# Optimization experiments

Hardware: AMD Instinct MI355X
Metric: run time of the kernel (lower is better)

Reference implementation:

```python
import jax, jax.numpy as jnp
import numpy as np


def setup_inputs() -> dict:
    key = jax.random.key(0)
    inputs = jax.random.normal(key, (32, 56, 56, 256), dtype=jnp.float32)
    return {"inputs": inputs, "n": 48}


def reference(inputs, n):
    # Flatten per batch row: [B, H*W*C]
    B = inputs.shape[0]
    flat = inputs.reshape(B, -1)
    # k-th largest value per row is the threshold
    values, _ = jax.lax.top_k(flat, n)
    thresholds = values[:, -1].reshape(B, 1, 1, 1)
    mask = (inputs >= thresholds).astype(inputs.dtype)
    return inputs * mask
```

## Files before the change

### kernel.cpp

```cpp
#include <hip/hip_runtime.h>
#include <stdint.h>

#define ROWS 32
#define ROW_LEN 802816
#define ROW_LEN4 200704
#define BPR 98
#define F4_PER_BLOCK 2048
#define THREADS 256
#define F4_PER_THREAD 8
#define TG 3.0f
#define BCAP 40
#define CAP_ROW (BPR * BCAP)
#define SLOTS_PT 16

#define OFF_BCNT 501760
#define OFF_THR  514304

__device__ __forceinline__ uint32_t fkey(float x) {
    uint32_t u = __float_as_uint(x);
    return (u & 0x80000000u) ? ~u : (u | 0x80000000u);
}
__device__ __forceinline__ float fkey_inv(uint32_t k) {
    uint32_t u = (k & 0x80000000u) ? (k & 0x7FFFFFFFu) : ~k;
    return __uint_as_float(u);
}

__global__ __launch_bounds__(THREADS) void k_spec(const float* __restrict__ in,
                                                  float* __restrict__ out,
                                                  uint32_t* __restrict__ pos,
                                                  int* __restrict__ bcnt) {
    __shared__ uint32_t lp[BCAP];
    __shared__ int lcnt;
    const int row = blockIdx.x / BPR;
    const int blk = blockIdx.x % BPR;
    if (threadIdx.x == 0) lcnt = 0;
    __syncthreads();
    const size_t base = (size_t)row * ROW_LEN4 + (size_t)blk * F4_PER_BLOCK + threadIdx.x;
    const float4* p = (const float4*)in + base;
    float4* q = (float4*)out + base;
    const float4 z = make_float4(0.f, 0.f, 0.f, 0.f);
#pragma unroll
    for (int v = 0; v < F4_PER_THREAD; ++v) {
        float4 d = p[v * THREADS];
        q[v * THREADS] = z;
        const uint32_t e = (uint32_t)(blk * F4_PER_BLOCK + v * THREADS + threadIdx.x) * 4u;
        if (d.x > TG) { int j = atomicAdd(&lcnt, 1); if (j < BCAP) lp[j] = e + 0u; }
        if (d.y > TG) { int j = atomicAdd(&lcnt, 1); if (j < BCAP) lp[j] = e + 1u; }
        if (d.z > TG) { int j = atomicAdd(&lcnt, 1); if (j < BCAP) lp[j] = e + 2u; }
        if (d.w > TG) { int j = atomicAdd(&lcnt, 1); if (j < BCAP) lp[j] = e + 3u; }
    }
    __syncthreads();
    const int c = lcnt;
    if (threadIdx.x == 0) bcnt[row * BPR + blk] = c;
    const int cc = c < BCAP ? c : BCAP;
    for (int i = threadIdx.x; i < cc; i += THREADS)
        pos[((size_t)row * BPR + blk) * BCAP + i] = lp[i];
}

__device__ __forceinline__ void pick_digit(uint32_t* h, int t, int r,
                                           int* sh_sel, int* sh_rank) {
#pragma unroll
    for (int off = 1; off < 256; off <<= 1) {
        uint32_t v = h[t] + ((t + off < 256) ? h[t + off] : 0u);
        __syncthreads();
        h[t] = v;
        __syncthreads();
    }
    const uint32_t Sd = h[t];
    const uint32_t Sd1 = (t < 255) ? h[t + 1] : 0u;
    if ((int)Sd >= r && (int)Sd1 < r) { *sh_sel = t; *sh_rank = r - (int)Sd1; }
    __syncthreads();
}

__global__ __launch_bounds__(THREADS) void k_sel(const float* __restrict__ in,
                                                 const int* __restrict__ n_ptr,
                                                 const int* __restrict__ bcnt,
                                                 const uint32_t* __restrict__ pos,
                                                 float* __restrict__ out,
                                                 float* __restrict__ thr) {
    __shared__ int lb[BPR];
    __shared__ uint32_t h[256];
    __shared__ int sh_sel, sh_rank, sh_m, sh_bad;
    const int row = blockIdx.x;
    const int t = threadIdx.x;
    const int n = *n_ptr;
    const float* rin = in + (size_t)row * ROW_LEN;
    float* rout = out + (size_t)row * ROW_LEN;

    if (t == 0) { sh_m = 0; sh_bad = 0; }
    __syncthreads();
    {
        int lsum = 0, lbad = 0;
        for (int b = t; b < BPR; b += THREADS) {
            const int c = bcnt[row * BPR + b];
            lbad |= (c > BCAP);
            const int cc = c < BCAP ? c : BCAP;
            lb[b] = cc;
            lsum += cc;
        }
        if (lsum) atomicAdd(&sh_m, lsum);
        if (lbad) atomicOr(&sh_bad, 1);
    }
    __syncthreads();
    const int m = sh_m;
    const bool ok = (!sh_bad) && (m >= n) && (n >= 1);

    if (ok) {
        uint32_t key[SLOTS_PT];
        uint32_t ps[SLOTS_PT];
        bool val[SLOTS_PT];
#pragma unroll
        for (int j = 0; j < SLOTS_PT; ++j) {
            const int slot = j * THREADS + t;
            uint32_t k = 0, pp = 0; bool v = false;
            if (slot < CAP_ROW) {
                const int b = slot / BCAP;
                v = (slot - b * BCAP) < lb[b];
                if (v) {
                    pp = pos[(size_t)row * CAP_ROW + slot];
                    k = fkey(rin[pp]);
                }
            }
            key[j] = k; ps[j] = pp; val[j] = v;
        }
        uint32_t prefix = 0, msk = 0;
        int r = n;
        for (int rd = 0; rd < 4; ++rd) {
            const int shn = 24 - rd * 8;
            h[t] = 0;
            __syncthreads();
#pragma unroll
            for (int j = 0; j < SLOTS_PT; ++j)
                if (val[j] && (key[j] & msk) == prefix)
                    atomicAdd(&h[(key[j] >> shn) & 255u], 1u);
            __syncthreads();
            pick_digit(h, t, r, &sh_sel, &sh_rank);
            prefix |= ((uint32_t)sh_sel) << shn;
            msk |= 255u << shn;
            r = sh_rank;
            __syncthreads();
        }
#pragma unroll
        for (int j = 0; j < SLOTS_PT; ++j)
            if (val[j] && key[j] >= prefix)
                rout[ps[j]] = fkey_inv(key[j]);
        if (t == 0) thr[row] = fkey_inv(prefix);
    } else {
        uint32_t prefix = 0, msk = 0;
        int r = (n < 1) ? 1 : n;
        const float4* p = (const float4*)rin;
        for (int rd = 0; rd < 4; ++rd) {
            const int shn = 24 - rd * 8;
            h[t] = 0;
            __syncthreads();
            for (int i = t; i < ROW_LEN4; i += THREADS) {
                const float4 d = p[i];
                uint32_t k;
                k = fkey(d.x); if ((k & msk) == prefix) atomicAdd(&h[(k >> shn) & 255u], 1u);
                k = fkey(d.y); if ((k & msk) == prefix) atomicAdd(&h[(k >> shn) & 255u], 1u);
                k = fkey(d.z); if ((k & msk) == prefix) atomicAdd(&h[(k >> shn) & 255u], 1u);
                k = fkey(d.w); if ((k & msk) == prefix) atomicAdd(&h[(k >> shn) & 255u], 1u);
            }
            __syncthreads();
            pick_digit(h, t, r, &sh_sel, &sh_rank);
            prefix |= ((uint32_t)sh_sel) << shn;
            msk |= 255u << shn;
            r = sh_rank;
            __syncthreads();
        }
        const float tf = fkey_inv(prefix);
        float4* q = (float4*)rout;
        for (int i = t; i < ROW_LEN4; i += THREADS) {
            float4 d = p[i];
            d.x = (d.x >= tf) ? d.x : 0.0f;
            d.y = (d.y >= tf) ? d.y : 0.0f;
            d.z = (d.z >= tf) ? d.z : 0.0f;
            d.w = (d.w >= tf) ? d.w : 0.0f;
            q[i] = d;
        }
        if (t == 0) thr[row] = tf;
    }
}

extern "C" void kernel_launch(void* const* d_in, const int* in_sizes, int n_in,
                              void* d_out, int out_size, void* d_ws, size_t ws_size,
                              hipStream_t stream) {
    const float* in = (const float*)d_in[0];
    const int* n_ptr = (const int*)d_in[1];
    float* out = (float*)d_out;
    char* ws = (char*)d_ws;

    uint32_t* pos = (uint32_t*)ws;
    int* bcnt = (int*)(ws + OFF_BCNT);
    float* thr = (float*)(ws + OFF_THR);

    k_spec<<<ROWS * BPR, THREADS, 0, stream>>>(in, out, pos, bcnt);
    k_sel<<<ROWS, THREADS, 0, stream>>>(in, n_ptr, bcnt, pos, out, thr);
}
```

Measured before the change: 50.32 us.

## Replace per-block candidate compaction with bitmask scan and per-row LDS gather

The scan kernel no longer uses LDS atomics to compact candidates above a fixed threshold. Each thread now records an 8-bit mask of which float4 pairs contain a value above the threshold, over larger tiles with half as many blocks per row. The select kernel reads these masks, re-reads only the flagged float4s from global memory, and compacts candidates into shared memory with a per-row cap of 2560 before the radix select. This takes the atomics and scattered position writes out of the bandwidth-bound pass. In exchange, the 32 select blocks do serialized mask walks and global re-reads, and use about 20KB of LDS each.

```diff
diff --git a/kernel.cpp b/kernel.cpp
--- a/kernel.cpp
+++ b/kernel.cpp
@@ -4,17 +4,17 @@
 #define ROWS 32
 #define ROW_LEN 802816
 #define ROW_LEN4 200704
-#define BPR 98
-#define F4_PER_BLOCK 2048
 #define THREADS 256
-#define F4_PER_THREAD 8
+
+#define SBPR 49
+#define TILE_F4 4096
+#define F4_PT 16
+#define SCAN_BLOCKS (ROWS * SBPR)
 #define TG 3.0f
-#define BCAP 40
-#define CAP_ROW (BPR * BCAP)
-#define SLOTS_PT 16
+#define CAP 2560
 
-#define OFF_BCNT 501760
-#define OFF_THR  514304
+
+typedef float f32x4 __attribute__((ext_vector_type(4)));
 
 __device__ __forceinline__ uint32_t fkey(float x) {
     uint32_t u = __float_as_uint(x);
@@ -25,36 +25,23 @@
     return __uint_as_float(u);
 }
 
-__global__ __launch_bounds__(THREADS) void k_spec(const float* __restrict__ in,
+__global__ __launch_bounds__(THREADS) void k_scan(const float* __restrict__ in,
                                                   float* __restrict__ out,
-                                                  uint32_t* __restrict__ pos,
-                                                  int* __restrict__ bcnt) {
-    __shared__ uint32_t lp[BCAP];
-    __shared__ int lcnt;
-    const int row = blockIdx.x / BPR;
-    const int blk = blockIdx.x % BPR;
-    if (threadIdx.x == 0) lcnt = 0;
-    __syncthreads();
-    const size_t base = (size_t)row * ROW_LEN4 + (size_t)blk * F4_PER_BLOCK + threadIdx.x;
+                                                  uint8_t* __restrict__ bm) {
+    const int bid = blockIdx.x;
+    const size_t base = (size_t)bid * TILE_F4 + threadIdx.x;
     const float4* p = (const float4*)in + base;
     float4* q = (float4*)out + base;
     const float4 z = make_float4(0.f, 0.f, 0.f, 0.f);
+    uint32_t cm = 0;
 #pragma unroll
-    for (int v = 0; v < F4_PER_THREAD; ++v) {
-        float4 d = p[v * THREADS];
-        q[v * THREADS] = z;
-        const uint32_t e = (uint32_t)(blk * F4_PER_BLOCK + v * THREADS + threadIdx.x) * 4u;
-        if (d.x > TG) { int j = atomicAdd(&lcnt, 1); if (j < BCAP) lp[j] = e + 0u; }
-        if (d.y > TG) { int j = atomicAdd(&lcnt, 1); if (j < BCAP) lp[j] = e + 1u; }
-        if (d.z > TG) { int j = atomicAdd(&lcnt, 1); if (j < BCAP) lp[j] = e + 2u; }
-        if (d.w > TG) { int j = atomicAdd(&lcnt, 1); if (j < BCAP) lp[j] = e + 3u; }
+    for (int it = 0; it < F4_PT; ++it) {
+        const float4 d = p[it * THREADS];
+        q[it * THREADS] = z;
+        const float mx = fmaxf(fmaxf(d.x, d.y), fmaxf(d.z, d.w));
+        cm |= (mx > TG) ? (1u << (it >> 1)) : 0u;
     }
-    __syncthreads();
-    const int c = lcnt;
-    if (threadIdx.x == 0) bcnt[row * BPR + blk] = c;
-    const int cc = c < BCAP ? c : BCAP;
-    for (int i = threadIdx.x; i < cc; i += THREADS)
-        pos[((size_t)row * BPR + blk) * BCAP + i] = lp[i];
+    bm[(size_t)bid * THREADS + threadIdx.x] = (uint8_t)cm;
 }
 
 __device__ __forceinline__ void pick_digit(uint32_t* h, int t, int r,
@@ -74,65 +61,54 @@
 
 __global__ __launch_bounds__(THREADS) void k_sel(const float* __restrict__ in,
                                                  const int* __restrict__ n_ptr,
-                                                 const int* __restrict__ bcnt,
-                                                 const uint32_t* __restrict__ pos,
-                                                 float* __restrict__ out,
-                                                 float* __restrict__ thr) {
-    __shared__ int lb[BPR];
+                                                 const uint8_t* __restrict__ bm,
+                                                 float* __restrict__ out) {
+    __shared__ uint32_t pos_l[CAP];
+    __shared__ uint32_t key_l[CAP];
     __shared__ uint32_t h[256];
-    __shared__ int sh_sel, sh_rank, sh_m, sh_bad;
+    __shared__ int sh_sel, sh_rank, sh_cnt;
     const int row = blockIdx.x;
     const int t = threadIdx.x;
     const int n = *n_ptr;
     const float* rin = in + (size_t)row * ROW_LEN;
     float* rout = out + (size_t)row * ROW_LEN;
+    const float4* rp = (const float4*)rin;
 
-    if (t == 0) { sh_m = 0; sh_bad = 0; }
+    if (t == 0) sh_cnt = 0;
     __syncthreads();
-    {
-        int lsum = 0, lbad = 0;
-        for (int b = t; b < BPR; b += THREADS) {
-            const int c = bcnt[row * BPR + b];
-            lbad |= (c > BCAP);
-            const int cc = c < BCAP ? c : BCAP;
-            lb[b] = cc;
-            lsum += cc;
+    for (int tl = 0; tl < SBPR; ++tl) {
+        uint32_t cm = bm[(size_t)(row * SBPR + tl) * THREADS + t];
+        while (cm) {
+            const int b = __builtin_ctz(cm);
+            cm &= cm - 1;
+#pragma unroll
+            for (int half = 0; half < 2; ++half) {
+                const uint32_t fi = (uint32_t)tl * TILE_F4
+                                    + (uint32_t)(2 * b + half) * THREADS + t;
+                const float4 d = rp[fi];
+                const uint32_t e = fi * 4u;
+                if (d.x > TG) { int j = atomicAdd(&sh_cnt, 1); if (j < CAP) { pos_l[j] = e + 0u; key_l[j] = fkey(d.x); } }
+                if (d.y > TG) { int j = atomicAdd(&sh_cnt, 1); if (j < CAP) { pos_l[j] = e + 1u; key_l[j] = fkey(d.y); } }
+                if (d.z > TG) { int j = atomicAdd(&sh_cnt, 1); if (j < CAP) { pos_l[j] = e + 2u; key_l[j] = fkey(d.z); } }
+                if (d.w > TG) { int j = atomicAdd(&sh_cnt, 1); if (j < CAP) { pos_l[j] = e + 3u; key_l[j] = fkey(d.w); } }
+            }
         }
-        if (lsum) atomicAdd(&sh_m, lsum);
-        if (lbad) atomicOr(&sh_bad, 1);
     }
     __syncthreads();
-    const int m = sh_m;
-    const bool ok = (!sh_bad) && (m >= n) && (n >= 1);
+    const int m = sh_cnt;
+    const bool ok = (m <= CAP) && (m >= n) && (n >= 1);
 
     if (ok) {
-        uint32_t key[SLOTS_PT];
-        uint32_t ps[SLOTS_PT];
-        bool val[SLOTS_PT];
-#pragma unroll
-        for (int j = 0; j < SLOTS_PT; ++j) {
-            const int slot = j * THREADS + t;
-            uint32_t k = 0, pp = 0; bool v = false;
-            if (slot < CAP_ROW) {
-                const int b = slot / BCAP;
-                v = (slot - b * BCAP) < lb[b];
-                if (v) {
-                    pp = pos[(size_t)row * CAP_ROW + slot];
-                    k = fkey(rin[pp]);
-                }
-            }
-            key[j] = k; ps[j] = pp; val[j] = v;
-        }
         uint32_t prefix = 0, msk = 0;
         int r = n;
         for (int rd = 0; rd < 4; ++rd) {
             const int shn = 24 - rd * 8;
             h[t] = 0;
             __syncthreads();
-#pragma unroll
-            for (int j = 0; j < SLOTS_PT; ++j)
-                if (val[j] && (key[j] & msk) == prefix)
-                    atomicAdd(&h[(key[j] >> shn) & 255u], 1u);
+            for (int i = t; i < m; i += THREADS) {
+                const uint32_t k = key_l[i];
+                if ((k & msk) == prefix) atomicAdd(&h[(k >> shn) & 255u], 1u);
+            }
             __syncthreads();
             pick_digit(h, t, r, &sh_sel, &sh_rank);
             prefix |= ((uint32_t)sh_sel) << shn;
@@ -140,21 +116,19 @@
             r = sh_rank;
             __syncthreads();
         }
-#pragma unroll
-        for (int j = 0; j < SLOTS_PT; ++j)
-            if (val[j] && key[j] >= prefix)
-                rout[ps[j]] = fkey_inv(key[j]);
-        if (t == 0) thr[row] = fkey_inv(prefix);
+        for (int i = t; i < m; i += THREADS) {
+            const uint32_t k = key_l[i];
+            if (k >= prefix) rout[pos_l[i]] = fkey_inv(k);
+        }
     } else {
         uint32_t prefix = 0, msk = 0;
         int r = (n < 1) ? 1 : n;
-        const float4* p = (const float4*)rin;
         for (int rd = 0; rd < 4; ++rd) {
             const int shn = 24 - rd * 8;
             h[t] = 0;
             __syncthreads();
             for (int i = t; i < ROW_LEN4; i += THREADS) {
-                const float4 d = p[i];
+                const float4 d = rp[i];
                 uint32_t k;
                 k = fkey(d.x); if ((k & msk) == prefix) atomicAdd(&h[(k >> shn) & 255u], 1u);
                 k = fkey(d.y); if ((k & msk) == prefix) atomicAdd(&h[(k >> shn) & 255u], 1u);
@@ -171,14 +145,13 @@
         const float tf = fkey_inv(prefix);
         float4* q = (float4*)rout;
         for (int i = t; i < ROW_LEN4; i += THREADS) {
-            float4 d = p[i];
+            float4 d = rp[i];
             d.x = (d.x >= tf) ? d.x : 0.0f;
             d.y = (d.y >= tf) ? d.y : 0.0f;
             d.z = (d.z >= tf) ? d.z : 0.0f;
             d.w = (d.w >= tf) ? d.w : 0.0f;
             q[i] = d;
         }
-        if (t == 0) thr[row] = tf;
     }
 }
 
@@ -188,12 +161,8 @@
     const float* in = (const float*)d_in[0];
     const int* n_ptr = (const int*)d_in[1];
     float* out = (float*)d_out;
-    char* ws = (char*)d_ws;
+    uint8_t* bm = (uint8_t*)d_ws;
 
-    uint32_t* pos = (uint32_t*)ws;
-    int* bcnt = (int*)(ws + OFF_BCNT);
-    float* thr = (float*)(ws + OFF_THR);
-
-    k_spec<<<ROWS * BPR, THREADS, 0, stream>>>(in, out, pos, bcnt);
-    k_sel<<<ROWS, THREADS, 0, stream>>>(in, n_ptr, bcnt, pos, out, thr);
+    k_scan<<<SCAN_BLOCKS, THREADS, 0, stream>>>(in, out, bm);
+    k_sel<<<ROWS, THREADS, 0, stream>>>(in, n_ptr, bm, out);
 }
```

After: 117.9 us. 134% more time.
